# Performance work log

Measured on AMD Instinct MI355X. Metric: run time of the kernel, lower is better.

## Reference

```python
import jax, jax.numpy as jnp
import numpy as np

D_MODEL = 1024
N_HEADS = 16
D_K = D_MODEL // N_HEADS
B, T = 4, 2048


def setup_inputs() -> dict:
    key = jax.random.key(0)
    ks = jax.random.split(key, 13)
    s = 1.0 / np.sqrt(D_MODEL)
    inp = {
        "Q": jax.random.normal(ks[0], (B, T, D_MODEL), jnp.float32),
        "K": jax.random.normal(ks[1], (B, T, D_MODEL), jnp.float32),
        "V": jax.random.normal(ks[2], (B, T, D_MODEL), jnp.float32),
        "mask": jax.random.randint(ks[3], (B, 1, 1, T), 0, 2, jnp.int32),
        "W_q": jax.random.normal(ks[4], (D_MODEL, D_MODEL), jnp.float32) * s,
        "b_q": jax.random.normal(ks[5], (D_MODEL,), jnp.float32) * s,
        "W_k": jax.random.normal(ks[6], (D_MODEL, D_MODEL), jnp.float32) * s,
        "b_k": jax.random.normal(ks[7], (D_MODEL,), jnp.float32) * s,
        "W_v": jax.random.normal(ks[8], (D_MODEL, D_MODEL), jnp.float32) * s,
        "b_v": jax.random.normal(ks[9], (D_MODEL,), jnp.float32) * s,
        "W_o": jax.random.normal(ks[10], (D_MODEL, D_MODEL), jnp.float32) * s,
        "b_o": jax.random.normal(ks[11], (D_MODEL,), jnp.float32) * s,
    }
    return inp


def _split_heads(x):
    # (B, T, d_model) -> (B, H, T, d_k)
    b, t, _ = x.shape
    return x.reshape(b, t, N_HEADS, D_K).transpose(0, 2, 1, 3)


def reference(Q, K, V, mask, W_q, b_q, W_k, b_k, W_v, b_v, W_o, b_o):
    # Linear projections (torch nn.Linear: x @ W.T + b)
    q = _split_heads(Q @ W_q.T + b_q)  # (B, H, T, d_k)
    k = _split_heads(K @ W_k.T + b_k)
    v = _split_heads(V @ W_v.T + b_v)

    scale = 1.0 / jnp.sqrt(jnp.asarray(D_K, q.dtype))
    scores = jnp.einsum('bhqd,bhkd->bhqk', q, k) * scale  # (B, H, T, T)
    scores = jnp.where(mask == 0, -jnp.inf, scores)
    attn = jax.nn.softmax(scores, axis=-1)
    out = jnp.einsum('bhqk,bhkd->bhqd', attn, v)  # (B, H, T, d_k)

    # combine heads: (B, H, T, d_k) -> (B, T, d_model)
    bsz, h, t, dk = out.shape
    out = out.transpose(0, 2, 1, 3).reshape(bsz, t, h * dk)
    return out @ W_o.T + b_o
```

## Files before the change

kernel.cpp:

```cpp
#include <hip/hip_runtime.h>
#include <hip/hip_bf16.h>
#include <stdint.h>

#define NHEADS 16
#define SEQ    2048
#define DMODEL 1024
#define DK     64

#define QB_OFF  0ull
#define KB_OFF  8388608ull
#define VB_OFF  16777216ull
#define WQ_OFF  25165824ull
#define WK_OFF  26214400ull
#define WV_OFF  27262976ull
#define WO_OFF  28311552ull
#define QH_OFF  29360128ull
#define KH_OFF  37748736ull
#define VT_OFF  46137344ull
#define MSKF_OFF 54525952ull
#define OC_OFF  0ull

typedef __attribute__((ext_vector_type(8))) __bf16 bf16x8;
typedef __attribute__((ext_vector_type(4))) float  floatx4;

__device__ __forceinline__ unsigned short f2bf(float f) {
  unsigned int u = __float_as_uint(f);
  u += 0x7fffu + ((u >> 16) & 1u);
  return (unsigned short)(u >> 16);
}

__device__ __forceinline__ unsigned int pk2(float hi, float lo) {
  return __builtin_amdgcn_perm(__float_as_uint(hi) + 0x8000u,
                               __float_as_uint(lo) + 0x8000u, 0x07060302u);
}

__device__ __forceinline__ void gld_lds16(const void* g, void* l) {
  __builtin_amdgcn_global_load_lds(
      (const __attribute__((address_space(1))) unsigned int*)(g),
      (__attribute__((address_space(3))) unsigned int*)(uintptr_t)(l),
      16, 0, 0);
}

struct CastArgs {
  const float* src[8];
  unsigned long long off[8];
  unsigned int n[8];
};

__global__ __launch_bounds__(256) void cast_bf16(CastArgs a, unsigned short* __restrict__ ws) {
  int ti = blockIdx.y;
  unsigned int n = a.n[ti];
  unsigned int stride = gridDim.x * blockDim.x * 4u;
  unsigned int i0 = (blockIdx.x * blockDim.x + threadIdx.x) * 4u;
  if (ti == 7) {
    const int* s = (const int*)a.src[7];
    float* d = (float*)(ws + a.off[7]);
    for (unsigned int i = i0; i < n; i += stride) {
      int4 v = *(const int4*)(s + i);
      float4 o = {(float)v.x, (float)v.y, (float)v.z, (float)v.w};
      *(float4*)(d + i) = o;
    }
    return;
  }
  const float* s = a.src[ti];
  unsigned short* d = ws + a.off[ti];
  for (unsigned int i = i0; i < n; i += stride) {
    float4 v = *(const float4*)(s + i);
    ushort4 o;
    o.x = f2bf(v.x); o.y = f2bf(v.y); o.z = f2bf(v.z); o.w = f2bf(v.w);
    *(ushort4*)(d + i) = o;
  }
}

__device__ __forceinline__ void gemm_core_128(
    const unsigned short* __restrict__ A, const unsigned short* __restrict__ Bw,
    int m0, int n0, unsigned short* As, unsigned short* Bs, floatx4 acc[4][4])
{
  int tid = threadIdx.x;
  int lane = tid & 63, l16 = lane & 15, quad = lane >> 4;
  int wave = tid >> 6, wm = wave >> 1, wn = wave & 1;
  #pragma unroll 1
  for (int kt = 0; kt < 32; ++kt) {
    __syncthreads();
    #pragma unroll
    for (int rnd = 0; rnd < 2; ++rnd) {
      int e = tid * 8 + rnd * 2048;
      int row = e >> 5, col = e & 31;
      gld_lds16(A  + (size_t)(m0 + row) * 1024 + kt * 32 + col, As + e);
      gld_lds16(Bw + (size_t)(n0 + row) * 1024 + kt * 32 + col, Bs + e);
    }
    __syncthreads();
    bf16x8 af[4], bfr[4];
    #pragma unroll
    for (int f = 0; f < 4; ++f) {
      af[f]  = *(const bf16x8*)(As + (wm * 64 + f * 16 + l16) * 32 + quad * 8);
      bfr[f] = *(const bf16x8*)(Bs + (wn * 64 + f * 16 + l16) * 32 + quad * 8);
    }
    #pragma unroll
    for (int fm = 0; fm < 4; ++fm)
      #pragma unroll
      for (int fn = 0; fn < 4; ++fn)
        acc[fm][fn] = __builtin_amdgcn_mfma_f32_16x16x32_bf16(af[fm], bfr[fn], acc[fm][fn], 0, 0, 0);
  }
}

__global__ __launch_bounds__(256) void proj_gemm(
    const unsigned short* __restrict__ wsc, unsigned short* __restrict__ ws,
    const float* __restrict__ bq, const float* __restrict__ bk, const float* __restrict__ bv)
{
  __shared__ unsigned short smem[17408];
  unsigned short* As = smem;
  unsigned short* Bs = smem + 4096;
  int z = blockIdx.z;
  int tid = threadIdx.x, lane = tid & 63, l16 = lane & 15, quad = lane >> 4;
  int wave = tid >> 6, wm = wave >> 1, wn = wave & 1;

  if (z < 2) {
    const unsigned short* A  = wsc + (z == 0 ? QB_OFF : KB_OFF);
    const unsigned short* Bw = wsc + (z == 0 ? WQ_OFF : WK_OFF);
    const float* bias = (z == 0) ? bq : bk;
    unsigned short* dst = ws + (z == 0 ? QH_OFF : KH_OFF);
    float scale = (z == 0) ? 0.18033688011111772f : 1.0f;

    int m0 = blockIdx.y * 128, n0 = blockIdx.x * 128;
    floatx4 acc[4][4] = {};
    gemm_core_128(A, Bw, m0, n0, As, Bs, acc);

    __syncthreads();
    #pragma unroll
    for (int fn = 0; fn < 4; ++fn) {
      int c = wn * 64 + fn * 16 + l16;
      float bvv = bias[n0 + c];
      #pragma unroll
      for (int fm = 0; fm < 4; ++fm)
        #pragma unroll
        for (int r = 0; r < 4; ++r) {
          int t = wm * 64 + fm * 16 + quad * 4 + r;
          smem[t * 136 + c] = f2bf((acc[fm][fn][r] + bvv) * scale);
        }
    }
    __syncthreads();
    #pragma unroll
    for (int it = 0; it < 8; ++it) {
      int e = it * 2048 + tid * 8;
      int t = e >> 7, c = e & 127;
      uint4 val = *(const uint4*)(smem + t * 136 + c);
      int m = m0 + t, b = m >> 11, tg = m & 2047;
      int h = (n0 + c) >> 6, d = (n0 + c) & 63;
      *(uint4*)(dst + ((size_t)(b * NHEADS + h) * SEQ + tg) * DK + d) = val;
    }
  } else {
    int flat = blockIdx.y * 8 + blockIdx.x;
    int b = flat >> 7, rem = flat & 127;
    int mt = rem >> 4, nt = rem & 15;
    int m0 = mt * 128, n0 = nt * 128;
    const unsigned short* A  = wsc + WV_OFF;
    const unsigned short* Bw = wsc + VB_OFF + (size_t)b * SEQ * DMODEL;
    unsigned short* dst = ws + VT_OFF;

    floatx4 acc[4][4] = {};
    gemm_core_128(A, Bw, m0, n0, As, Bs, acc);

    __syncthreads();
    #pragma unroll
    for (int fm = 0; fm < 4; ++fm) {
      int mb = m0 + wm * 64 + fm * 16 + quad * 4;
      float4 bb4 = *(const float4*)(bv + mb);
      float bbv[4] = {bb4.x, bb4.y, bb4.z, bb4.w};
      #pragma unroll
      for (int r = 0; r < 4; ++r) {
        int mrow = wm * 64 + fm * 16 + quad * 4 + r;
        #pragma unroll
        for (int fn = 0; fn < 4; ++fn) {
          int t = wn * 64 + fn * 16 + l16;
          int tp = (t & ~31) | ((t & 12) << 1) | ((t & 16) >> 2) | (t & 3);
          smem[mrow * 136 + tp] = f2bf(acc[fm][fn][r] + bbv[r]);
        }
      }
    }
    __syncthreads();
    #pragma unroll
    for (int it = 0; it < 8; ++it) {
      int e = it * 2048 + tid * 8;
      int mrow = e >> 7, tcol = e & 127;
      uint4 val = *(const uint4*)(smem + mrow * 136 + tcol);
      int m = m0 + mrow, h = m >> 6, d = m & 63;
      *(uint4*)(dst + ((size_t)(b * NHEADS + h) * DK + d) * SEQ + n0 + tcol) = val;
    }
  }
}

__global__ __launch_bounds__(128, 2) void attn_fused(
    const unsigned short* __restrict__ wsc, unsigned short* __restrict__ ws)
{
  __shared__ unsigned short smem[16640];
  unsigned short* Ks  = smem;
  unsigned short* Vts = smem + 8192;
  float* MskF = (float*)(smem + 16384);

  int qt = blockIdx.x, bh = blockIdx.y;
  int b = bh >> 4, h = bh & 15;
  int tid = threadIdx.x, wave = tid >> 6, lane = tid & 63, l16 = lane & 15, quad = lane >> 4;
  int wq = wave * 64;

  const unsigned short* qh = wsc + QH_OFF + (size_t)bh * SEQ * DK;
  const unsigned short* kh = wsc + KH_OFF + (size_t)bh * SEQ * DK;
  const unsigned short* vt = wsc + VT_OFF + (size_t)bh * DK * SEQ;
  const float* mkf = (const float*)(wsc + MSKF_OFF) + b * SEQ;

  #pragma unroll
  for (int kk = 0; kk < 2; ++kk)
    #pragma unroll
    for (int rnd = 0; rnd < 4; ++rnd) {
      int e = tid * 8 + rnd * 1024;
      int row = e >> 5, col = e & 31;
      gld_lds16(qh + (size_t)(qt * 128 + row) * DK + kk * 32 + col, Ks + kk * 4096 + e);
    }
  __syncthreads();
  bf16x8 qf[4][2];
  #pragma unroll
  for (int fq = 0; fq < 4; ++fq)
    #pragma unroll
    for (int kk = 0; kk < 2; ++kk)
      qf[fq][kk] = *(const bf16x8*)(Ks + kk * 4096 + (wq + fq * 16 + l16) * 32 + quad * 8);

  float rsum[4] = {0.f, 0.f, 0.f, 0.f};
  floatx4 o[4][4] = {};
  const floatx4 zero4 = {};

  #pragma unroll 1
  for (int jt = 0; jt < 16; ++jt) {
    __syncthreads();
    #pragma unroll
    for (int kk = 0; kk < 2; ++kk)
      #pragma unroll
      for (int rnd = 0; rnd < 4; ++rnd) {
        int e = tid * 8 + rnd * 1024;
        int row = e >> 5, col = e & 31;
        gld_lds16(kh + (size_t)(jt * 128 + row) * DK + kk * 32 + col, Ks + kk * 4096 + e);
      }
    #pragma unroll
    for (int kk = 0; kk < 4; ++kk)
      #pragma unroll
      for (int rnd = 0; rnd < 2; ++rnd) {
        int e = tid * 8 + rnd * 1024;
        int row = e >> 5, col = e & 31;
        gld_lds16(vt + (size_t)row * SEQ + jt * 128 + kk * 32 + col, Vts + kk * 2048 + e);
      }
    if (tid < 32)
      gld_lds16(mkf + jt * 128 + tid * 4, (char*)MskF + tid * 16);
    __syncthreads();

    #pragma unroll
    for (int w = 0; w < 4; ++w) {
      floatx4 s[2][4];
      #pragma unroll
      for (int f2 = 0; f2 < 2; ++f2) {
        int fk = 2 * w + f2;
        bf16x8 kf0 = *(const bf16x8*)(Ks +        (fk * 16 + l16) * 32 + quad * 8);
        bf16x8 kf1 = *(const bf16x8*)(Ks + 4096 + (fk * 16 + l16) * 32 + quad * 8);
        #pragma unroll
        for (int fq = 0; fq < 4; ++fq) {
          s[f2][fq] = __builtin_amdgcn_mfma_f32_16x16x32_bf16(kf0, qf[fq][0], zero4, 0, 0, 0);
          s[f2][fq] = __builtin_amdgcn_mfma_f32_16x16x32_bf16(kf1, qf[fq][1], s[f2][fq], 0, 0, 0);
        }
      }
      #pragma unroll
      for (int f2 = 0; f2 < 2; ++f2) {
        float4 m4 = *(const float4*)(MskF + (2 * w + f2) * 16 + quad * 4);
        float mf[4] = {m4.x, m4.y, m4.z, m4.w};
        #pragma unroll
        for (int fq = 0; fq < 4; ++fq)
          #pragma unroll
          for (int r = 0; r < 4; ++r) {
            float p = __builtin_amdgcn_exp2f(s[f2][fq][r]) * mf[r];
            s[f2][fq][r] = p;
            rsum[fq] += p;
          }
      }
      union { unsigned int u[4]; bf16x8 v; } pf[4];
      #pragma unroll
      for (int fq = 0; fq < 4; ++fq) {
        pf[fq].u[0] = pk2(s[0][fq][1], s[0][fq][0]);
        pf[fq].u[1] = pk2(s[0][fq][3], s[0][fq][2]);
        pf[fq].u[2] = pk2(s[1][fq][1], s[1][fq][0]);
        pf[fq].u[3] = pk2(s[1][fq][3], s[1][fq][2]);
      }
      #pragma unroll
      for (int fd = 0; fd < 4; ++fd) {
        bf16x8 vf = *(const bf16x8*)(Vts + w * 2048 + (fd * 16 + l16) * 32 + quad * 8);
        #pragma unroll
        for (int fq = 0; fq < 4; ++fq)
          o[fd][fq] = __builtin_amdgcn_mfma_f32_16x16x32_bf16(vf, pf[fq].v, o[fd][fq], 0, 0, 0);
      }
    }
  }

  float inv[4];
  #pragma unroll
  for (int fq = 0; fq < 4; ++fq) {
    float rs = rsum[fq];
    rs += __shfl_xor(rs, 16, 64);
    rs += __shfl_xor(rs, 32, 64);
    inv[fq] = __builtin_amdgcn_rcpf(rs);
  }
  __syncthreads();
  unsigned short* Ot = smem;
  #pragma unroll
  for (int fd = 0; fd < 4; ++fd)
    #pragma unroll
    for (int fq = 0; fq < 4; ++fq)
      #pragma unroll
      for (int r = 0; r < 4; ++r) {
        int q = wq + fq * 16 + l16;
        int d = fd * 16 + quad * 4 + r;
        Ot[q * 72 + d] = f2bf(o[fd][fq][r] * inv[fq]);
      }
  __syncthreads();
  unsigned short* oc = ws + OC_OFF;
  #pragma unroll
  for (int rr = 0; rr < 8; ++rr) {
    int e = rr * 1024 + tid * 8;
    int q = e >> 6, off = e & 63;
    uint4 val = *(const uint4*)(Ot + q * 72 + off);
    *(uint4*)(oc + ((size_t)(b * SEQ + qt * 128 + q)) * DMODEL + h * DK + off) = val;
  }
}

__global__ __launch_bounds__(256) void out_gemm(
    const unsigned short* __restrict__ wsc, const float* __restrict__ bo,
    float* __restrict__ out)
{
  __shared__ unsigned short smem[8192];
  unsigned short* As = smem;
  unsigned short* Bs = smem + 4096;
  int m0 = blockIdx.y * 128, n0 = blockIdx.x * 128;
  floatx4 acc[4][4] = {};
  gemm_core_128(wsc + OC_OFF, wsc + WO_OFF, m0, n0, As, Bs, acc);

  int tid = threadIdx.x, lane = tid & 63, l16 = lane & 15, quad = lane >> 4;
  int wave = tid >> 6, wm = wave >> 1, wn = wave & 1;
  #pragma unroll
  for (int fn = 0; fn < 4; ++fn) {
    int n = n0 + wn * 64 + fn * 16 + l16;
    float bvv = bo[n];
    #pragma unroll
    for (int fm = 0; fm < 4; ++fm)
      #pragma unroll
      for (int r = 0; r < 4; ++r) {
        int m = m0 + wm * 64 + fm * 16 + quad * 4 + r;
        out[(size_t)m * DMODEL + n] = acc[fm][fn][r] + bvv;
      }
  }
}

extern "C" void kernel_launch(void* const* d_in, const int* in_sizes, int n_in,
                              void* d_out, int out_size, void* d_ws, size_t ws_size,
                              hipStream_t stream) {
  const float* Q    = (const float*)d_in[0];
  const float* K    = (const float*)d_in[1];
  const float* V    = (const float*)d_in[2];
  const float* bq   = (const float*)d_in[5];
  const float* bk   = (const float*)d_in[7];
  const float* bv   = (const float*)d_in[9];
  const float* bo   = (const float*)d_in[11];
  unsigned short* ws = (unsigned short*)d_ws;
  float* out = (float*)d_out;

  CastArgs ca;
  ca.src[0] = Q;  ca.src[1] = K;  ca.src[2] = V;
  ca.src[3] = (const float*)d_in[4]; ca.src[4] = (const float*)d_in[6];
  ca.src[5] = (const float*)d_in[8]; ca.src[6] = (const float*)d_in[10];
  ca.src[7] = (const float*)d_in[3];
  ca.off[0] = QB_OFF; ca.off[1] = KB_OFF; ca.off[2] = VB_OFF;
  ca.off[3] = WQ_OFF; ca.off[4] = WK_OFF; ca.off[5] = WV_OFF; ca.off[6] = WO_OFF;
  ca.off[7] = MSKF_OFF;
  ca.n[0] = ca.n[1] = ca.n[2] = 8388608u;
  ca.n[3] = ca.n[4] = ca.n[5] = ca.n[6] = 1048576u;
  ca.n[7] = 8192u;

  hipLaunchKernelGGL(cast_bf16, dim3(2048, 8), dim3(256), 0, stream, ca, ws);
  hipLaunchKernelGGL(proj_gemm, dim3(8, 64, 3), dim3(256), 0, stream, ws, ws, bq, bk, bv);
  hipLaunchKernelGGL(attn_fused, dim3(16, 64), dim3(128), 0, stream, ws, ws);
  hipLaunchKernelGGL(out_gemm, dim3(8, 64), dim3(256), 0, stream, ws, bo, out);
}
```

Baseline: 356.1 us.

## Fold key mask into V projection and compute row sums via MFMA

```diff
diff --git a/kernel.cpp b/kernel.cpp
--- a/kernel.cpp
+++ b/kernel.cpp
@@ -29,11 +29,6 @@
   return (unsigned short)(u >> 16);
 }
 
-__device__ __forceinline__ unsigned int pk2(float hi, float lo) {
-  return __builtin_amdgcn_perm(__float_as_uint(hi) + 0x8000u,
-                               __float_as_uint(lo) + 0x8000u, 0x07060302u);
-}
-
 __device__ __forceinline__ void gld_lds16(const void* g, void* l) {
   __builtin_amdgcn_global_load_lds(
       (const __attribute__((address_space(1))) unsigned int*)(g),
@@ -54,11 +49,16 @@
   unsigned int i0 = (blockIdx.x * blockDim.x + threadIdx.x) * 4u;
   if (ti == 7) {
     const int* s = (const int*)a.src[7];
-    float* d = (float*)(ws + a.off[7]);
+    unsigned short* d = ws + a.off[7];
     for (unsigned int i = i0; i < n; i += stride) {
       int4 v = *(const int4*)(s + i);
-      float4 o = {(float)v.x, (float)v.y, (float)v.z, (float)v.w};
-      *(float4*)(d + i) = o;
+      ushort4 o;
+      o.x = v.x ? 0x3f80u : 0u;
+      o.y = v.y ? 0x3f80u : 0u;
+      o.z = v.z ? 0x3f80u : 0u;
+      o.w = v.w ? 0x3f80u : 0u;
+      unsigned int p = (i & ~31u) | ((i & 12u) << 1) | ((i & 16u) >> 2) | (i & 3u);
+      *(ushort4*)(d + p) = o;
     }
     return;
   }
@@ -161,6 +161,17 @@
     floatx4 acc[4][4] = {};
     gemm_core_128(A, Bw, m0, n0, As, Bs, acc);
 
+    const unsigned short* pm = wsc + MSKF_OFF + (size_t)b * SEQ;
+    int tpl[4];
+    float mv[4];
+    #pragma unroll
+    for (int fn = 0; fn < 4; ++fn) {
+      int t = wn * 64 + fn * 16 + l16;
+      int tp = (t & ~31) | ((t & 12) << 1) | ((t & 16) >> 2) | (t & 3);
+      tpl[fn] = tp;
+      mv[fn] = __uint_as_float((unsigned int)pm[n0 + tp] << 16);
+    }
+
     __syncthreads();
     #pragma unroll
     for (int fm = 0; fm < 4; ++fm) {
@@ -171,11 +182,8 @@
       for (int r = 0; r < 4; ++r) {
         int mrow = wm * 64 + fm * 16 + quad * 4 + r;
         #pragma unroll
-        for (int fn = 0; fn < 4; ++fn) {
-          int t = wn * 64 + fn * 16 + l16;
-          int tp = (t & ~31) | ((t & 12) << 1) | ((t & 16) >> 2) | (t & 3);
-          smem[mrow * 136 + tp] = f2bf(acc[fm][fn][r] + bbv[r]);
-        }
+        for (int fn = 0; fn < 4; ++fn)
+          smem[mrow * 136 + tpl[fn]] = f2bf((acc[fm][fn][r] + bbv[r]) * mv[fn]);
       }
     }
     __syncthreads();
@@ -196,7 +204,7 @@
   __shared__ unsigned short smem[16640];
   unsigned short* Ks  = smem;
   unsigned short* Vts = smem + 8192;
-  float* MskF = (float*)(smem + 16384);
+  unsigned short* MskB = smem + 16384;
 
   int qt = blockIdx.x, bh = blockIdx.y;
   int b = bh >> 4, h = bh & 15;
@@ -206,7 +214,7 @@
   const unsigned short* qh = wsc + QH_OFF + (size_t)bh * SEQ * DK;
   const unsigned short* kh = wsc + KH_OFF + (size_t)bh * SEQ * DK;
   const unsigned short* vt = wsc + VT_OFF + (size_t)bh * DK * SEQ;
-  const float* mkf = (const float*)(wsc + MSKF_OFF) + b * SEQ;
+  const unsigned short* pm = wsc + MSKF_OFF + (size_t)b * SEQ;
 
   #pragma unroll
   for (int kk = 0; kk < 2; ++kk)
@@ -224,8 +232,8 @@
     for (int kk = 0; kk < 2; ++kk)
       qf[fq][kk] = *(const bf16x8*)(Ks + kk * 4096 + (wq + fq * 16 + l16) * 32 + quad * 8);
 
-  float rsum[4] = {0.f, 0.f, 0.f, 0.f};
   floatx4 o[4][4] = {};
+  floatx4 osum[4] = {};
   const floatx4 zero4 = {};
 
   #pragma unroll 1
@@ -247,8 +255,8 @@
         int row = e >> 5, col = e & 31;
         gld_lds16(vt + (size_t)row * SEQ + jt * 128 + kk * 32 + col, Vts + kk * 2048 + e);
       }
-    if (tid < 32)
-      gld_lds16(mkf + jt * 128 + tid * 4, (char*)MskF + tid * 16);
+    if (tid < 16)
+      gld_lds16(pm + jt * 128 + tid * 8, MskB + tid * 8);
     __syncthreads();
 
     #pragma unroll
@@ -266,26 +274,27 @@
         }
       }
       #pragma unroll
-      for (int f2 = 0; f2 < 2; ++f2) {
-        float4 m4 = *(const float4*)(MskF + (2 * w + f2) * 16 + quad * 4);
-        float mf[4] = {m4.x, m4.y, m4.z, m4.w};
+      for (int f2 = 0; f2 < 2; ++f2)
         #pragma unroll
         for (int fq = 0; fq < 4; ++fq)
           #pragma unroll
-          for (int r = 0; r < 4; ++r) {
-            float p = __builtin_amdgcn_exp2f(s[f2][fq][r]) * mf[r];
-            s[f2][fq][r] = p;
-            rsum[fq] += p;
-          }
-      }
+          for (int r = 0; r < 4; ++r)
+            s[f2][fq][r] = __builtin_amdgcn_exp2f(s[f2][fq][r]);
+
       union { unsigned int u[4]; bf16x8 v; } pf[4];
       #pragma unroll
       for (int fq = 0; fq < 4; ++fq) {
-        pf[fq].u[0] = pk2(s[0][fq][1], s[0][fq][0]);
-        pf[fq].u[1] = pk2(s[0][fq][3], s[0][fq][2]);
-        pf[fq].u[2] = pk2(s[1][fq][1], s[1][fq][0]);
-        pf[fq].u[3] = pk2(s[1][fq][3], s[1][fq][2]);
-      }
+        asm("v_cvt_pk_bf16_f32 %0, %1, %2" : "=v"(pf[fq].u[0]) : "v"(s[0][fq][0]), "v"(s[0][fq][1]));
+        asm("v_cvt_pk_bf16_f32 %0, %1, %2" : "=v"(pf[fq].u[1]) : "v"(s[0][fq][2]), "v"(s[0][fq][3]));
+        asm("v_cvt_pk_bf16_f32 %0, %1, %2" : "=v"(pf[fq].u[2]) : "v"(s[1][fq][0]), "v"(s[1][fq][1]));
+        asm("v_cvt_pk_bf16_f32 %0, %1, %2" : "=v"(pf[fq].u[3]) : "v"(s[1][fq][2]), "v"(s[1][fq][3]));
+      }
+
+      bf16x8 mvf = *(const bf16x8*)(MskB + w * 32 + quad * 8);
+      #pragma unroll
+      for (int fq = 0; fq < 4; ++fq)
+        osum[fq] = __builtin_amdgcn_mfma_f32_16x16x32_bf16(mvf, pf[fq].v, osum[fq], 0, 0, 0);
+
       #pragma unroll
       for (int fd = 0; fd < 4; ++fd) {
         bf16x8 vf = *(const bf16x8*)(Vts + w * 2048 + (fd * 16 + l16) * 32 + quad * 8);
@@ -298,12 +307,9 @@
 
   float inv[4];
   #pragma unroll
-  for (int fq = 0; fq < 4; ++fq) {
-    float rs = rsum[fq];
-    rs += __shfl_xor(rs, 16, 64);
-    rs += __shfl_xor(rs, 32, 64);
-    inv[fq] = __builtin_amdgcn_rcpf(rs);
-  }
+  for (int fq = 0; fq < 4; ++fq)
+    inv[fq] = __builtin_amdgcn_rcpf(osum[fq][0]);
+
   __syncthreads();
   unsigned short* Ot = smem;
   #pragma unroll
```

Result: faster. 344.5 us (-3.3%).
